# Kernel tuning notes

Measured on AMD Instinct MI355X. Metric: run time of the kernel, lower is better.

## Reference

```python
import jax, jax.numpy as jnp
import numpy as np

BETA = 0.9
THRESHOLD = 1.0
SURROGATE_K = 25.0  # superspike slope

@jax.custom_vjp
def spike(u):
    # Heaviside forward, superspike surrogate gradient
    return (u > 0).astype(u.dtype)

def _spike_fwd(u):
    return spike(u), u

def _spike_bwd(u, g):
    return (g / jnp.square(1.0 + SURROGATE_K * jnp.abs(u)),)

spike.defvjp(_spike_fwd, _spike_bwd)

T, B = 512, 256
VIS_D, IMU_D, TRAJ_D = 256, 64, 64
HID, OUT = 256, 128
FUSE = VIS_D + IMU_D + TRAJ_D  # 384

def setup_inputs() -> dict:
    key = jax.random.key(0)
    ks = jax.random.split(key, 8)
    s_in = 1.0 / np.sqrt(FUSE)
    s_h = 1.0 / np.sqrt(HID)
    return {
        "vis_seq": jax.random.normal(ks[0], (T, B, VIS_D), jnp.float32),
        "imu_seq": jax.random.normal(ks[1], (T, B, IMU_D), jnp.float32),
        "traj_seq": jax.random.normal(ks[2], (T, B, TRAJ_D), jnp.float32),
        "W_in": jax.random.normal(ks[3], (FUSE, HID), jnp.float32) * s_in,
        "b_in": jnp.zeros((HID,), jnp.float32),
        "w_rec": jax.random.normal(ks[4], (HID,), jnp.float32) * 0.1,  # RLIF elementwise recurrent weight
        "W_head": jax.random.normal(ks[5], (HID, OUT), jnp.float32) * s_h,
        "b_head": jnp.zeros((OUT,), jnp.float32),
    }

def reference(vis_seq, imu_seq, traj_seq, W_in, b_in, w_rec, W_head, b_head):
    # fuse latents: [T, B, FUSE]
    fuse_seq = jnp.concatenate([vis_seq, imu_seq, traj_seq], axis=-1)
    # in_proj is time-invariant -> hoist the GEMM out of the scan (same math)
    x_proj = jnp.einsum("tbf,fh->tbh", fuse_seq, W_in) + b_in  # [T, B, HID]
    batch = imu_seq.shape[1]
    V0 = jnp.zeros((batch, HID), x_proj.dtype)
    S0 = jnp.zeros((batch, HID), x_proj.dtype)

    def step(carry, x_t):
        V, S = carry
        # recurrent LIF: leak + input + elementwise recurrent spike feedback
        V = BETA * V + x_t + w_rec * S
        S_new = spike(V - THRESHOLD)
        V = V - S_new * THRESHOLD  # soft reset
        return (V, S_new), S_new

    _, spikes_seq = jax.lax.scan(step, (V0, S0), x_proj)  # [T, B, HID]
    # head is also time-invariant -> single GEMM over the whole sequence
    logits_seq = jnp.einsum("tbh,ho->tbo", spikes_seq, W_head) + b_head  # [T, B, OUT]
    out = jnp.mean(logits_seq, axis=0)  # readout='mean' over time
    return out, logits_seq
```

## Files before the change

kernel.cpp:

```cpp
#include <hip/hip_runtime.h>
#include <hip/hip_bf16.h>
#include <cstdint>

#define T_LEN 512
#define B_SZ  256
#define HID   256
#define OUT   128
#define FUSE  384
#define MROWS (T_LEN * B_SZ)
#define FT    64

typedef _Float16 f16x8 __attribute__((ext_vector_type(8)));
typedef float f32x4 __attribute__((ext_vector_type(4)));

#define PRESC 4096.0f
#define S1    2048.0f
#define S1INV 4.8828125e-4f
#define C0    5.9604644775390625e-8f

#define EPSV  5e-5f

__global__ __launch_bounds__(256) void prep_win(const float* __restrict__ Win,
                                                _Float16* __restrict__ Bpack)
{
  int id = blockIdx.x * 256 + threadIdx.x;
  int img = id >> 10;
  int c = img >> 1, bc = img & 1;
  int slot = id & 1023;
  int s = slot >> 9, sub = (slot >> 6) & 7, pos = slot & 63;
  int fr = pos & 15, fq = pos >> 4;
  int n = bc * 128 + sub * 16 + fr;
  int k0 = c * 32 + fq * 8;
  f16x8 v;
#pragma unroll
  for (int j = 0; j < 8; ++j) {
    float w = Win[(size_t)(k0 + j) * HID + n] * PRESC;
    _Float16 h = (_Float16)w;
    v[j] = (s == 0) ? h : (_Float16)((w - (float)h) * S1);
  }
  *reinterpret_cast<f16x8*>(&Bpack[(size_t)img * 8192 + slot * 8]) = v;
}

__global__ __launch_bounds__(256) void prep_whead(const float* __restrict__ Wh,
                                                  _Float16* __restrict__ Wh3)
{
  int id = blockIdx.x * 256 + threadIdx.x;
  int n = id & 127, kk = (id >> 7) & 31, c = id >> 12;
  Wh3[((size_t)c * 128 + n) * 32 + kk] = (_Float16)Wh[(c * 32 + kk) * OUT + n];
}

__global__ __launch_bounds__(512, 4) void k12_fused(
    const float* __restrict__ vis, const float* __restrict__ imu,
    const float* __restrict__ traj, const _Float16* __restrict__ Bpack,
    const float* __restrict__ bin, const float* __restrict__ wrec,
    uint32_t* __restrict__ sbits, float* __restrict__ scnt)
{
  __shared__ __align__(16) _Float16 Asl[2][4096];
  __shared__ float xt[FT][130];

  const int bid = blockIdx.x;
  const int b   = bid & 255;
  const int hh  = bid >> 8;
  const int tid = threadIdx.x;
  const int wid = tid >> 6, lane = tid & 63;
  const int wr = wid >> 2, wc = wid & 3;
  const int fr = lane & 15, fq = lane >> 4;

  const int arow = (wid & 3) * 16 + fr;
  const int ak   = fq * 8;

  float V = 0.f, S = 0.f, cnt = 0.f, minm = 1e9f;
  const float wrv = (tid < 128) ? wrec[hh * 128 + tid] : 0.f;
  float bvv[2];
  bvv[0] = bin[hh * 128 + wc * 32 + fr];
  bvv[1] = bin[hh * 128 + wc * 32 + 16 + fr];

  float4 a0, a1;
  f16x8 pb0, pb1, pb2, pb3;

  auto loadA = [&](int tc, int c) {
    if (tid < 256) {
      size_t m = (size_t)(tc * FT + arow) * B_SZ + b;
      const float* src; size_t off;
      if (c < 8)       { src = vis;  off = m * 256 + c * 32 + ak; }
      else if (c < 10) { src = imu;  off = m * 64 + (c - 8) * 32 + ak; }
      else             { src = traj; off = m * 64 + (c - 10) * 32 + ak; }
      a0 = *reinterpret_cast<const float4*>(src + off);
      a1 = *reinterpret_cast<const float4*>(src + off + 4);
    }
  };
  auto loadB = [&](int c) {
    const _Float16* base = Bpack + (size_t)(c * 2 + hh) * 8192;
    pb0 = *reinterpret_cast<const f16x8*>(base + (wc * 2 + 0) * 512 + lane * 8);
    pb1 = *reinterpret_cast<const f16x8*>(base + (wc * 2 + 1) * 512 + lane * 8);
    pb2 = *reinterpret_cast<const f16x8*>(base + 4096 + (wc * 2 + 0) * 512 + lane * 8);
    pb3 = *reinterpret_cast<const f16x8*>(base + 4096 + (wc * 2 + 1) * 512 + lane * 8);
  };

  loadA(0, 0); loadB(0);

  for (int tc = 0; tc < 8; ++tc) {
    f32x4 acc0[2][2] = {};
    f32x4 acc1[2][2] = {};

#pragma unroll 1
    for (int c = 0; c < 12; ++c) {
      _Float16* buf = &Asl[c & 1][0];
      if (tid < 256) {
        float av[8] = {a0.x, a0.y, a0.z, a0.w, a1.x, a1.y, a1.z, a1.w};
        f16x8 vh, vl;
#pragma unroll
        for (int j = 0; j < 8; ++j) {
          float w = av[j] * PRESC;
          _Float16 h = (_Float16)w;
          vh[j] = h;
          vl[j] = (_Float16)((w - (float)h) * S1);
        }
        *reinterpret_cast<f16x8*>(&buf[tid * 8])        = vh;
        *reinterpret_cast<f16x8*>(&buf[2048 + tid * 8]) = vl;
      }
      __syncthreads();
      f16x8 bh_0 = pb0, bh_1 = pb1, bl_0 = pb2, bl_1 = pb3;
      if (c + 1 < 12)      { loadA(tc, c + 1); loadB(c + 1); }
      else if (tc + 1 < 8) { loadA(tc + 1, 0); loadB(0); }

#pragma unroll
      for (int mf = 0; mf < 2; ++mf) {
        int sa = wr * 2 + mf;
        f16x8 ah = *reinterpret_cast<const f16x8*>(&buf[sa * 512 + lane * 8]);
        f16x8 al = *reinterpret_cast<const f16x8*>(&buf[2048 + sa * 512 + lane * 8]);
        acc0[mf][0] = __builtin_amdgcn_mfma_f32_16x16x32_f16(ah, bh_0, acc0[mf][0], 0, 0, 0);
        acc1[mf][0] = __builtin_amdgcn_mfma_f32_16x16x32_f16(ah, bl_0, acc1[mf][0], 0, 0, 0);
        acc1[mf][0] = __builtin_amdgcn_mfma_f32_16x16x32_f16(al, bh_0, acc1[mf][0], 0, 0, 0);
        acc0[mf][1] = __builtin_amdgcn_mfma_f32_16x16x32_f16(ah, bh_1, acc0[mf][1], 0, 0, 0);
        acc1[mf][1] = __builtin_amdgcn_mfma_f32_16x16x32_f16(ah, bl_1, acc1[mf][1], 0, 0, 0);
        acc1[mf][1] = __builtin_amdgcn_mfma_f32_16x16x32_f16(al, bh_1, acc1[mf][1], 0, 0, 0);
      }
    }
    __syncthreads();

#pragma unroll
    for (int mf = 0; mf < 2; ++mf)
#pragma unroll
      for (int nf = 0; nf < 2; ++nf) {
        int col = wc * 32 + nf * 16 + fr;
        int rbase = wr * 32 + mf * 16 + fq * 4;
#pragma unroll
        for (int r = 0; r < 4; ++r)
          xt[rbase + r][col] =
              (acc0[mf][nf][r] + acc1[mf][nf][r] * S1INV) * C0 + bvv[nf];
      }
    __syncthreads();

    if (tid < 128) {
#pragma unroll 1
      for (int u0 = 0; u0 < FT; u0 += 8) {
        float xv[8];
#pragma unroll
        for (int u = 0; u < 8; ++u) xv[u] = xt[u0 + u][tid];
#pragma unroll
        for (int u = 0; u < 8; ++u) {
          V = 0.9f * V + xv[u] + wrv * S;
          float d = V - 1.0f;
          float sn = (d > 0.0f) ? 1.0f : 0.0f;
          minm = fminf(minm, fabsf(d));
          V -= sn;
          cnt += sn;
          S = sn;
          unsigned long long mk = __ballot(sn > 0.5f);
          if (lane == 0) {
            int m = (tc * FT + u0 + u) * B_SZ + b;
            int wv = hh * 2 + wid;
            sbits[(size_t)m * 8 + wv * 2 + 0] = (uint32_t)(mk & 0xffffffffull);
            sbits[(size_t)m * 8 + wv * 2 + 1] = (uint32_t)(mk >> 32);
          }
        }
      }
    }
  }

  if (tid < 128)
    scnt[b * HID + hh * 128 + tid] = (minm < EPSV) ? (-cnt - 1.0f) : cnt;
}

#define FSL 12
__global__ __launch_bounds__(512) void k2_fix(
    const float* __restrict__ vis, const float* __restrict__ imu,
    const float* __restrict__ traj, const float* __restrict__ Win,
    const float* __restrict__ bin, const float* __restrict__ wrec,
    uint32_t* __restrict__ sbits, float* __restrict__ scnt)
{
  __shared__ __align__(16) float Wlds[FSL][392];
  __shared__ float xcol[FSL][521];
  __shared__ unsigned char spkb[FSL][516];
  __shared__ int dlist[256];
  __shared__ int nd;

  const int b = blockIdx.x;
  const int tid = threadIdx.x;
  if (tid == 0) nd = 0;
  __syncthreads();
  if (tid < 256) {
    if (scnt[b * HID + tid] < -0.5f) {
      int p = atomicAdd(&nd, 1);
      dlist[p] = tid;
    }
  }
  __syncthreads();
  const int nd0 = nd;
  if (nd0 == 0) return;

  const int t = tid;
  const size_t r = (size_t)t * B_SZ + b;

  for (int sb = 0; sb < nd0; sb += FSL) {
    const int nsb = min(FSL, nd0 - sb);

    for (int idx = tid; idx < FSL * 384; idx += 512) {
      int s = idx / 384, k = idx - s * 384;
      float w = 0.f;
      if (s < nsb) w = Win[(size_t)k * HID + dlist[sb + s]];
      Wlds[s][k] = w;
    }
    __syncthreads();

    float x[FSL];
#pragma unroll
    for (int s = 0; s < FSL; ++s) x[s] = 0.f;

#define SEG(SRC, LEN, DIM, WOFS)                                              \
    {                                                                         \
      const float* src = SRC + r * DIM;                                       \
      _Pragma("unroll 1")                                                     \
      for (int q = 0; q < LEN; q += 4) {                                      \
        float4 a0 = *reinterpret_cast<const float4*>(src + q * 4);            \
        float4 a1 = *reinterpret_cast<const float4*>(src + q * 4 + 4);        \
        float4 a2 = *reinterpret_cast<const float4*>(src + q * 4 + 8);        \
        float4 a3 = *reinterpret_cast<const float4*>(src + q * 4 + 12);       \
        _Pragma("unroll")                                                     \
        for (int s = 0; s < FSL; ++s) {                                       \
          float4 w = *reinterpret_cast<const float4*>(&Wlds[s][WOFS + q * 4]);\
          x[s] += a0.x * w.x; x[s] += a0.y * w.y;                             \
          x[s] += a0.z * w.z; x[s] += a0.w * w.w;                             \
        }                                                                     \
        _Pragma("unroll")                                                     \
        for (int s = 0; s < FSL; ++s) {                                       \
          float4 w = *reinterpret_cast<const float4*>(&Wlds[s][WOFS + q * 4 + 4]); \
          x[s] += a1.x * w.x; x[s] += a1.y * w.y;                             \
          x[s] += a1.z * w.z; x[s] += a1.w * w.w;                             \
        }                                                                     \
        _Pragma("unroll")                                                     \
        for (int s = 0; s < FSL; ++s) {                                       \
          float4 w = *reinterpret_cast<const float4*>(&Wlds[s][WOFS + q * 4 + 8]); \
          x[s] += a2.x * w.x; x[s] += a2.y * w.y;                             \
          x[s] += a2.z * w.z; x[s] += a2.w * w.w;                             \
        }                                                                     \
        _Pragma("unroll")                                                     \
        for (int s = 0; s < FSL; ++s) {                                       \
          float4 w = *reinterpret_cast<const float4*>(&Wlds[s][WOFS + q * 4 + 12]); \
          x[s] += a3.x * w.x; x[s] += a3.y * w.y;                             \
          x[s] += a3.z * w.z; x[s] += a3.w * w.w;                             \
        }                                                                     \
      }                                                                       \
    }

    SEG(vis,  64, 256, 0)
    SEG(imu,  16, 64,  256)
    SEG(traj, 16, 64,  320)
#undef SEG

#pragma unroll
    for (int s = 0; s < FSL; ++s) {
      if (s < nsb) xcol[s][t] = x[s] + bin[dlist[sb + s]];
    }
    __syncthreads();

    if (tid < nsb) {
      const int h = dlist[sb + tid];
      const float mywr = wrec[h];
      float V = 0.f, Sv = 0.f, cnt = 0.f;
#pragma unroll 1
      for (int tt = 0; tt < T_LEN; ++tt) {
        float xv = xcol[tid][tt];
        V = 0.9f * V + xv + mywr * Sv;
        float sn = (V - 1.0f > 0.0f) ? 1.0f : 0.0f;
        V -= sn;
        cnt += sn;
        Sv = sn;
        spkb[tid][tt] = (unsigned char)sn;
      }
      scnt[b * HID + h] = cnt;
    }
    __syncthreads();

    for (int p = tid; p < T_LEN * 8; p += 512) {
      int tt = p >> 3, wv = p & 7;
      uint32_t mc = 0, ms = 0;
      for (int j = 0; j < nsb; ++j) {
        int h = dlist[sb + j];
        if ((h >> 5) == wv) {
          uint32_t bit = 1u << (h & 31);
          mc |= bit;
          if (spkb[j][tt]) ms |= bit;
        }
      }
      if (mc) {
        size_t w = ((size_t)tt * B_SZ + b) * 8 + wv;
        sbits[w] = (sbits[w] & ~mc) | ms;
      }
    }
    __syncthreads();
  }
}

#define LDA 40
__global__ __launch_bounds__(256) void k3_logits(
    const uint32_t* __restrict__ sbits, const _Float16* __restrict__ Wh3,
    const float* __restrict__ bhead, float* __restrict__ logits)
{
  __shared__ __align__(16) _Float16 Sa[128][LDA];
  __shared__ __align__(16) _Float16 Wt[128][LDA];

  const int tid  = threadIdx.x;
  const int brow = blockIdx.x * 128;
  const int srow = tid >> 1, sks = (tid & 1) << 4;
  const int wid = tid >> 6, lane = tid & 63;
  const int wr = wid >> 1, wc = wid & 1;
  const int fr = lane & 15, fq = lane >> 4;

  f32x4 acc[4][4] = {};
  uint32_t wbits;
  uint4 wb0, wb1;

  auto loadS = [&](int c) { wbits = sbits[(size_t)(brow + srow) * 8 + c]; };
  auto loadW = [&](int c) {
    const _Float16* p = Wh3 + ((size_t)c * 128 + srow) * 32 + sks;
    wb0 = *reinterpret_cast<const uint4*>(p);
    wb1 = *reinterpret_cast<const uint4*>(p + 8);
  };

  loadS(0); loadW(0);

  for (int c = 0; c < 8; ++c) {
    __syncthreads();
    {
      f16x8 e0, e1;
#pragma unroll
      for (int j = 0; j < 8; ++j) {
        e0[j] = (_Float16)(float)((wbits >> (sks + j)) & 1u);
        e1[j] = (_Float16)(float)((wbits >> (sks + 8 + j)) & 1u);
      }
      *reinterpret_cast<f16x8*>(&Sa[srow][sks])     = e0;
      *reinterpret_cast<f16x8*>(&Sa[srow][sks + 8]) = e1;
    }
    *reinterpret_cast<uint4*>(&Wt[srow][sks])     = wb0;
    *reinterpret_cast<uint4*>(&Wt[srow][sks + 8]) = wb1;
    __syncthreads();
    if (c + 1 < 8) { loadS(c + 1); loadW(c + 1); }

    f16x8 wf[4];
#pragma unroll
    for (int nf = 0; nf < 4; ++nf)
      wf[nf] = *reinterpret_cast<const f16x8*>(&Wt[wc * 64 + nf * 16 + fr][fq * 8]);
#pragma unroll
    for (int mf = 0; mf < 4; ++mf) {
      f16x8 sf = *reinterpret_cast<const f16x8*>(&Sa[wr * 64 + mf * 16 + fr][fq * 8]);
#pragma unroll
      for (int nf = 0; nf < 4; ++nf)
        acc[mf][nf] = __builtin_amdgcn_mfma_f32_16x16x32_f16(sf, wf[nf], acc[mf][nf], 0, 0, 0);
    }
  }

#pragma unroll
  for (int mf = 0; mf < 4; ++mf)
#pragma unroll
    for (int nf = 0; nf < 4; ++nf) {
      int n = wc * 64 + nf * 16 + fr;
      float bv = bhead[n];
#pragma unroll
      for (int r = 0; r < 4; ++r) {
        int m = brow + wr * 64 + mf * 16 + fq * 4 + r;
        logits[(size_t)m * OUT + n] = acc[mf][nf][r] + bv;
      }
    }
}

__global__ __launch_bounds__(128) void k4_out(
    const float* __restrict__ scnt, const float* __restrict__ Whead,
    const float* __restrict__ bhead, float* __restrict__ outp)
{
  __shared__ float s[HID];
  const int b = blockIdx.x;
  const int o = threadIdx.x;
  s[o] = scnt[b * HID + o];
  s[o + 128] = scnt[b * HID + o + 128];
  __syncthreads();
  float acc = 0.f;
#pragma unroll 8
  for (int h = 0; h < HID; ++h) acc += s[h] * Whead[h * OUT + o];
  outp[b * OUT + o] = acc * (1.0f / (float)T_LEN) + bhead[o];
}

extern "C" void kernel_launch(void* const* d_in, const int* in_sizes, int n_in,
                              void* d_out, int out_size, void* d_ws, size_t ws_size,
                              hipStream_t stream)
{
  const float* vis   = (const float*)d_in[0];
  const float* imu   = (const float*)d_in[1];
  const float* traj  = (const float*)d_in[2];
  const float* Win   = (const float*)d_in[3];
  const float* bin   = (const float*)d_in[4];
  const float* wrec  = (const float*)d_in[5];
  const float* Whead = (const float*)d_in[6];
  const float* bhead = (const float*)d_in[7];

  float* outp   = (float*)d_out;
  float* logits = outp + B_SZ * OUT;

  char* ws = (char*)d_ws;
  const size_t SBITS_B = (size_t)MROWS * 8 * 4;
  const size_t SCNT_B  = (size_t)B_SZ * HID * 4;
  const size_t BPACK_B = (size_t)24 * 8192 * 2;
  uint32_t* sbits = (uint32_t*)ws;
  float*    scnt  = (float*)(ws + SBITS_B);
  _Float16* Bpack = (_Float16*)(ws + SBITS_B + SCNT_B);
  _Float16* Wh3   = (_Float16*)(ws + SBITS_B + SCNT_B + BPACK_B);

  prep_win  <<<dim3(24576 / 256), 256, 0, stream>>>(Win, Bpack);
  prep_whead<<<dim3(32768 / 256), 256, 0, stream>>>(Whead, Wh3);
  k12_fused <<<dim3(512),         512, 0, stream>>>(vis, imu, traj, Bpack, bin,
                                                    wrec, sbits, scnt);
  k2_fix    <<<dim3(B_SZ),        512, 0, stream>>>(vis, imu, traj, Win, bin,
                                                    wrec, sbits, scnt);
  k3_logits <<<dim3(MROWS / 128), 256, 0, stream>>>(sbits, Wh3, bhead, logits);
  k4_out    <<<dim3(B_SZ),        128, 0, stream>>>(scnt, Whead, bhead, outp);
}
```

Measured before the change: 284.3 us.

## Split A-tile staging across two thread groups with two-chunk-deep prefetch

```diff
diff --git a/kernel.cpp b/kernel.cpp
--- a/kernel.cpp
+++ b/kernel.cpp
@@ -63,10 +63,12 @@
   const int hh  = bid >> 8;
   const int tid = threadIdx.x;
   const int wid = tid >> 6, lane = tid & 63;
+  const int grp = tid >> 8;
+  const int stid = tid & 255;
   const int wr = wid >> 2, wc = wid & 3;
   const int fr = lane & 15, fq = lane >> 4;
 
-  const int arow = (wid & 3) * 16 + fr;
+  const int arow = (stid >> 6) * 16 + fr;
   const int ak   = fq * 8;
 
   float V = 0.f, S = 0.f, cnt = 0.f, minm = 1e9f;
@@ -78,18 +80,18 @@
   float4 a0, a1;
   f16x8 pb0, pb1, pb2, pb3;
 
-  auto loadA = [&](int tc, int c) {
-    if (tid < 256) {
-      size_t m = (size_t)(tc * FT + arow) * B_SZ + b;
-      const float* src; size_t off;
-      if (c < 8)       { src = vis;  off = m * 256 + c * 32 + ak; }
-      else if (c < 10) { src = imu;  off = m * 64 + (c - 8) * 32 + ak; }
-      else             { src = traj; off = m * 64 + (c - 10) * 32 + ak; }
-      a0 = *reinterpret_cast<const float4*>(src + off);
-      a1 = *reinterpret_cast<const float4*>(src + off + 4);
-    }
+  auto loadA = [&](int cc) {
+    int tcc = cc / 12, c = cc - tcc * 12;
+    size_t m = (size_t)(tcc * FT + arow) * B_SZ + b;
+    const float* src; size_t off;
+    if (c < 8)       { src = vis;  off = m * 256 + c * 32 + ak; }
+    else if (c < 10) { src = imu;  off = m * 64 + (c - 8) * 32 + ak; }
+    else             { src = traj; off = m * 64 + (c - 10) * 32 + ak; }
+    a0 = *reinterpret_cast<const float4*>(src + off);
+    a1 = *reinterpret_cast<const float4*>(src + off + 4);
   };
-  auto loadB = [&](int c) {
+  auto loadB = [&](int cc) {
+    int c = cc - (cc / 12) * 12;
     const _Float16* base = Bpack + (size_t)(c * 2 + hh) * 8192;
     pb0 = *reinterpret_cast<const f16x8*>(base + (wc * 2 + 0) * 512 + lane * 8);
     pb1 = *reinterpret_cast<const f16x8*>(base + (wc * 2 + 1) * 512 + lane * 8);
@@ -97,82 +99,87 @@
     pb3 = *reinterpret_cast<const f16x8*>(base + 4096 + (wc * 2 + 1) * 512 + lane * 8);
   };
 
-  loadA(0, 0); loadB(0);
-
-  for (int tc = 0; tc < 8; ++tc) {
-    f32x4 acc0[2][2] = {};
-    f32x4 acc1[2][2] = {};
+  loadA(grp);
+  loadB(0);
+
+  f32x4 acc0[2][2] = {};
+  f32x4 acc1[2][2] = {};
 
 #pragma unroll 1
-    for (int c = 0; c < 12; ++c) {
-      _Float16* buf = &Asl[c & 1][0];
-      if (tid < 256) {
-        float av[8] = {a0.x, a0.y, a0.z, a0.w, a1.x, a1.y, a1.z, a1.w};
-        f16x8 vh, vl;
-#pragma unroll
-        for (int j = 0; j < 8; ++j) {
-          float w = av[j] * PRESC;
-          _Float16 h = (_Float16)w;
-          vh[j] = h;
-          vl[j] = (_Float16)((w - (float)h) * S1);
+  for (int cc = 0; cc < 96; ++cc) {
+    _Float16* buf = &Asl[cc & 1][0];
+    const bool mine = (grp == (cc & 1));
+    if (mine) {
+      float av[8] = {a0.x, a0.y, a0.z, a0.w, a1.x, a1.y, a1.z, a1.w};
+      f16x8 vh, vl;
+#pragma unroll
+      for (int j = 0; j < 8; ++j) {
+        float w = av[j] * PRESC;
+        _Float16 h = (_Float16)w;
+        vh[j] = h;
+        vl[j] = (_Float16)((w - (float)h) * S1);
+      }
+      *reinterpret_cast<f16x8*>(&buf[stid * 8])        = vh;
+      *reinterpret_cast<f16x8*>(&buf[2048 + stid * 8]) = vl;
+    }
+    __syncthreads();
+    f16x8 bh_0 = pb0, bh_1 = pb1, bl_0 = pb2, bl_1 = pb3;
+    if (mine && cc + 2 < 96) loadA(cc + 2);
+    if (cc + 1 < 96) loadB(cc + 1);
+
+#pragma unroll
+    for (int mf = 0; mf < 2; ++mf) {
+      int sa = wr * 2 + mf;
+      f16x8 ah = *reinterpret_cast<const f16x8*>(&buf[sa * 512 + lane * 8]);
+      f16x8 al = *reinterpret_cast<const f16x8*>(&buf[2048 + sa * 512 + lane * 8]);
+      acc0[mf][0] = __builtin_amdgcn_mfma_f32_16x16x32_f16(ah, bh_0, acc0[mf][0], 0, 0, 0);
+      acc1[mf][0] = __builtin_amdgcn_mfma_f32_16x16x32_f16(ah, bl_0, acc1[mf][0], 0, 0, 0);
+      acc1[mf][0] = __builtin_amdgcn_mfma_f32_16x16x32_f16(al, bh_0, acc1[mf][0], 0, 0, 0);
+      acc0[mf][1] = __builtin_amdgcn_mfma_f32_16x16x32_f16(ah, bh_1, acc0[mf][1], 0, 0, 0);
+      acc1[mf][1] = __builtin_amdgcn_mfma_f32_16x16x32_f16(ah, bl_1, acc1[mf][1], 0, 0, 0);
+      acc1[mf][1] = __builtin_amdgcn_mfma_f32_16x16x32_f16(al, bh_1, acc1[mf][1], 0, 0, 0);
+    }
+
+    if ((cc - (cc / 12) * 12) == 11) {
+      const int tc = cc / 12;
+      __syncthreads();
+#pragma unroll
+      for (int mf = 0; mf < 2; ++mf)
+#pragma unroll
+        for (int nf = 0; nf < 2; ++nf) {
+          int col = wc * 32 + nf * 16 + fr;
+          int rbase = wr * 32 + mf * 16 + fq * 4;
+#pragma unroll
+          for (int r = 0; r < 4; ++r)
+            xt[rbase + r][col] =
+                (acc0[mf][nf][r] + acc1[mf][nf][r] * S1INV) * C0 + bvv[nf];
+          acc0[mf][nf] = (f32x4){0.f, 0.f, 0.f, 0.f};
+          acc1[mf][nf] = (f32x4){0.f, 0.f, 0.f, 0.f};
         }
-        *reinterpret_cast<f16x8*>(&buf[tid * 8])        = vh;
-        *reinterpret_cast<f16x8*>(&buf[2048 + tid * 8]) = vl;
-      }
       __syncthreads();
-      f16x8 bh_0 = pb0, bh_1 = pb1, bl_0 = pb2, bl_1 = pb3;
-      if (c + 1 < 12)      { loadA(tc, c + 1); loadB(c + 1); }
-      else if (tc + 1 < 8) { loadA(tc + 1, 0); loadB(0); }
-
-#pragma unroll
-      for (int mf = 0; mf < 2; ++mf) {
-        int sa = wr * 2 + mf;
-        f16x8 ah = *reinterpret_cast<const f16x8*>(&buf[sa * 512 + lane * 8]);
-        f16x8 al = *reinterpret_cast<const f16x8*>(&buf[2048 + sa * 512 + lane * 8]);
-        acc0[mf][0] = __builtin_amdgcn_mfma_f32_16x16x32_f16(ah, bh_0, acc0[mf][0], 0, 0, 0);
-        acc1[mf][0] = __builtin_amdgcn_mfma_f32_16x16x32_f16(ah, bl_0, acc1[mf][0], 0, 0, 0);
-        acc1[mf][0] = __builtin_amdgcn_mfma_f32_16x16x32_f16(al, bh_0, acc1[mf][0], 0, 0, 0);
-        acc0[mf][1] = __builtin_amdgcn_mfma_f32_16x16x32_f16(ah, bh_1, acc0[mf][1], 0, 0, 0);
-        acc1[mf][1] = __builtin_amdgcn_mfma_f32_16x16x32_f16(ah, bl_1, acc1[mf][1], 0, 0, 0);
-        acc1[mf][1] = __builtin_amdgcn_mfma_f32_16x16x32_f16(al, bh_1, acc1[mf][1], 0, 0, 0);
-      }
-    }
-    __syncthreads();
-
-#pragma unroll
-    for (int mf = 0; mf < 2; ++mf)
-#pragma unroll
-      for (int nf = 0; nf < 2; ++nf) {
-        int col = wc * 32 + nf * 16 + fr;
-        int rbase = wr * 32 + mf * 16 + fq * 4;
-#pragma unroll
-        for (int r = 0; r < 4; ++r)
-          xt[rbase + r][col] =
-              (acc0[mf][nf][r] + acc1[mf][nf][r] * S1INV) * C0 + bvv[nf];
-      }
-    __syncthreads();
-
-    if (tid < 128) {
+
+      if (tid < 128) {
 #pragma unroll 1
-      for (int u0 = 0; u0 < FT; u0 += 8) {
-        float xv[8];
-#pragma unroll
-        for (int u = 0; u < 8; ++u) xv[u] = xt[u0 + u][tid];
-#pragma unroll
-        for (int u = 0; u < 8; ++u) {
-          V = 0.9f * V + xv[u] + wrv * S;
-          float d = V - 1.0f;
-          float sn = (d > 0.0f) ? 1.0f : 0.0f;
-          minm = fminf(minm, fabsf(d));
-          V -= sn;
-          cnt += sn;
-          S = sn;
-          unsigned long long mk = __ballot(sn > 0.5f);
-          if (lane == 0) {
-            int m = (tc * FT + u0 + u) * B_SZ + b;
-            int wv = hh * 2 + wid;
-            sbits[(size_t)m * 8 + wv * 2 + 0] = (uint32_t)(mk & 0xffffffffull);
-            sbits[(size_t)m * 8 + wv * 2 + 1] = (uint32_t)(mk >> 32);
+        for (int u0 = 0; u0 < FT; u0 += 8) {
+          float xv[8];
+#pragma unroll
+          for (int u = 0; u < 8; ++u) xv[u] = xt[u0 + u][tid];
+#pragma unroll
+          for (int u = 0; u < 8; ++u) {
+            V = 0.9f * V + xv[u] + wrv * S;
+            float d = V - 1.0f;
+            float sn = (d > 0.0f) ? 1.0f : 0.0f;
+            minm = fminf(minm, fabsf(d));
+            V -= sn;
+            cnt += sn;
+            S = sn;
+            unsigned long long mk = __ballot(sn > 0.5f);
+            if (lane == 0) {
+              int m = (tc * FT + u0 + u) * B_SZ + b;
+              int wv = hh * 2 + wid;
+              sbits[(size_t)m * 8 + wv * 2 + 0] = (uint32_t)(mk & 0xffffffffull);
+              sbits[(size_t)m * 8 + wv * 2 + 1] = (uint32_t)(mk >> 32);
+            }
           }
         }
       }
```

New measurement: 277.9 us. -2.2%, faster.

## Use all 512 threads to stage two K-chunks per barrier in fused GEMM

Applied to the files above, without the earlier changes.

```diff
diff --git a/kernel.cpp b/kernel.cpp
--- a/kernel.cpp
+++ b/kernel.cpp
@@ -55,7 +55,7 @@
     const float* __restrict__ bin, const float* __restrict__ wrec,
     uint32_t* __restrict__ sbits, float* __restrict__ scnt)
 {
-  __shared__ __align__(16) _Float16 Asl[2][4096];
+  __shared__ __align__(16) _Float16 Asl[2][8192];
   __shared__ float xt[FT][130];
 
   const int bid = blockIdx.x;
@@ -63,11 +63,13 @@
   const int hh  = bid >> 8;
   const int tid = threadIdx.x;
   const int wid = tid >> 6, lane = tid & 63;
+  const int img  = tid >> 8;
+  const int stid = tid & 255;
   const int wr = wid >> 2, wc = wid & 3;
   const int fr = lane & 15, fq = lane >> 4;
 
-  const int arow = (wid & 3) * 16 + fr;
-  const int ak   = fq * 8;
+  const int arow = (stid >> 6) * 16 + (stid & 15);
+  const int ak   = ((stid & 63) >> 4) * 8;
 
   float V = 0.f, S = 0.f, cnt = 0.f, minm = 1e9f;
   const float wrv = (tid < 128) ? wrec[hh * 128 + tid] : 0.f;
@@ -76,37 +78,39 @@
   bvv[1] = bin[hh * 128 + wc * 32 + 16 + fr];
 
   float4 a0, a1;
-  f16x8 pb0, pb1, pb2, pb3;
+  f16x8 pb[2][4];
 
   auto loadA = [&](int tc, int c) {
-    if (tid < 256) {
-      size_t m = (size_t)(tc * FT + arow) * B_SZ + b;
-      const float* src; size_t off;
-      if (c < 8)       { src = vis;  off = m * 256 + c * 32 + ak; }
-      else if (c < 10) { src = imu;  off = m * 64 + (c - 8) * 32 + ak; }
-      else             { src = traj; off = m * 64 + (c - 10) * 32 + ak; }
-      a0 = *reinterpret_cast<const float4*>(src + off);
-      a1 = *reinterpret_cast<const float4*>(src + off + 4);
-    }
+    size_t m = (size_t)(tc * FT + arow) * B_SZ + b;
+    const float* src; size_t off;
+    if (c < 8)       { src = vis;  off = m * 256 + c * 32 + ak; }
+    else if (c < 10) { src = imu;  off = m * 64 + (c - 8) * 32 + ak; }
+    else             { src = traj; off = m * 64 + (c - 10) * 32 + ak; }
+    a0 = *reinterpret_cast<const float4*>(src + off);
+    a1 = *reinterpret_cast<const float4*>(src + off + 4);
   };
-  auto loadB = [&](int c) {
-    const _Float16* base = Bpack + (size_t)(c * 2 + hh) * 8192;
-    pb0 = *reinterpret_cast<const f16x8*>(base + (wc * 2 + 0) * 512 + lane * 8);
-    pb1 = *reinterpret_cast<const f16x8*>(base + (wc * 2 + 1) * 512 + lane * 8);
-    pb2 = *reinterpret_cast<const f16x8*>(base + 4096 + (wc * 2 + 0) * 512 + lane * 8);
-    pb3 = *reinterpret_cast<const f16x8*>(base + 4096 + (wc * 2 + 1) * 512 + lane * 8);
+  auto loadB = [&](int i) {
+#pragma unroll
+    for (int ii = 0; ii < 2; ++ii) {
+      const _Float16* base = Bpack + (size_t)((2 * i + ii) * 2 + hh) * 8192;
+      pb[ii][0] = *reinterpret_cast<const f16x8*>(base + (wc * 2 + 0) * 512 + lane * 8);
+      pb[ii][1] = *reinterpret_cast<const f16x8*>(base + (wc * 2 + 1) * 512 + lane * 8);
+      pb[ii][2] = *reinterpret_cast<const f16x8*>(base + 4096 + (wc * 2 + 0) * 512 + lane * 8);
+      pb[ii][3] = *reinterpret_cast<const f16x8*>(base + 4096 + (wc * 2 + 1) * 512 + lane * 8);
+    }
   };
 
-  loadA(0, 0); loadB(0);
+  loadA(0, img);
+  loadB(0);
+
+  f32x4 acc0[2][2] = {};
+  f32x4 acc1[2][2] = {};
 
   for (int tc = 0; tc < 8; ++tc) {
-    f32x4 acc0[2][2] = {};
-    f32x4 acc1[2][2] = {};
-
 #pragma unroll 1
-    for (int c = 0; c < 12; ++c) {
-      _Float16* buf = &Asl[c & 1][0];
-      if (tid < 256) {
+    for (int i = 0; i < 6; ++i) {
+      _Float16* buf = &Asl[i & 1][0];
+      {
         float av[8] = {a0.x, a0.y, a0.z, a0.w, a1.x, a1.y, a1.z, a1.w};
         f16x8 vh, vl;
 #pragma unroll
@@ -116,26 +120,29 @@
           vh[j] = h;
           vl[j] = (_Float16)((w - (float)h) * S1);
         }
-        *reinterpret_cast<f16x8*>(&buf[tid * 8])        = vh;
-        *reinterpret_cast<f16x8*>(&buf[2048 + tid * 8]) = vl;
+        *reinterpret_cast<f16x8*>(&buf[img * 4096 + stid * 8])        = vh;
+        *reinterpret_cast<f16x8*>(&buf[img * 4096 + 2048 + stid * 8]) = vl;
       }
       __syncthreads();
-      f16x8 bh_0 = pb0, bh_1 = pb1, bl_0 = pb2, bl_1 = pb3;
-      if (c + 1 < 12)      { loadA(tc, c + 1); loadB(c + 1); }
-      else if (tc + 1 < 8) { loadA(tc + 1, 0); loadB(0); }
-
-#pragma unroll
-      for (int mf = 0; mf < 2; ++mf) {
-        int sa = wr * 2 + mf;
-        f16x8 ah = *reinterpret_cast<const f16x8*>(&buf[sa * 512 + lane * 8]);
-        f16x8 al = *reinterpret_cast<const f16x8*>(&buf[2048 + sa * 512 + lane * 8]);
-        acc0[mf][0] = __builtin_amdgcn_mfma_f32_16x16x32_f16(ah, bh_0, acc0[mf][0], 0, 0, 0);
-        acc1[mf][0] = __builtin_amdgcn_mfma_f32_16x16x32_f16(ah, bl_0, acc1[mf][0], 0, 0, 0);
-        acc1[mf][0] = __builtin_amdgcn_mfma_f32_16x16x32_f16(al, bh_0, acc1[mf][0], 0, 0, 0);
-        acc0[mf][1] = __builtin_amdgcn_mfma_f32_16x16x32_f16(ah, bh_1, acc0[mf][1], 0, 0, 0);
-        acc1[mf][1] = __builtin_amdgcn_mfma_f32_16x16x32_f16(ah, bl_1, acc1[mf][1], 0, 0, 0);
-        acc1[mf][1] = __builtin_amdgcn_mfma_f32_16x16x32_f16(al, bh_1, acc1[mf][1], 0, 0, 0);
-      }
+
+#pragma unroll
+      for (int ii = 0; ii < 2; ++ii) {
+#pragma unroll
+        for (int mf = 0; mf < 2; ++mf) {
+          int sa = wr * 2 + mf;
+          f16x8 ah = *reinterpret_cast<const f16x8*>(&buf[ii * 4096 + sa * 512 + lane * 8]);
+          f16x8 al = *reinterpret_cast<const f16x8*>(&buf[ii * 4096 + 2048 + sa * 512 + lane * 8]);
+          acc0[mf][0] = __builtin_amdgcn_mfma_f32_16x16x32_f16(ah, pb[ii][0], acc0[mf][0], 0, 0, 0);
+          acc1[mf][0] = __builtin_amdgcn_mfma_f32_16x16x32_f16(ah, pb[ii][2], acc1[mf][0], 0, 0, 0);
+          acc1[mf][0] = __builtin_amdgcn_mfma_f32_16x16x32_f16(al, pb[ii][0], acc1[mf][0], 0, 0, 0);
+          acc0[mf][1] = __builtin_amdgcn_mfma_f32_16x16x32_f16(ah, pb[ii][1], acc0[mf][1], 0, 0, 0);
+          acc1[mf][1] = __builtin_amdgcn_mfma_f32_16x16x32_f16(ah, pb[ii][3], acc1[mf][1], 0, 0, 0);
+          acc1[mf][1] = __builtin_amdgcn_mfma_f32_16x16x32_f16(al, pb[ii][1], acc1[mf][1], 0, 0, 0);
+        }
+      }
+
+      if (i + 1 < 6)       { loadA(tc, 2 * (i + 1) + img); loadB(i + 1); }
+      else if (tc + 1 < 8) { loadA(tc + 1, img);           loadB(0); }
     }
     __syncthreads();
 
@@ -149,6 +156,8 @@
         for (int r = 0; r < 4; ++r)
           xt[rbase + r][col] =
               (acc0[mf][nf][r] + acc1[mf][nf][r] * S1INV) * C0 + bvv[nf];
+        acc0[mf][nf] = (f32x4){0.f, 0.f, 0.f, 0.f};
+        acc1[mf][nf] = (f32x4){0.f, 0.f, 0.f, 0.f};
       }
     __syncthreads();
 
```

New measurement: 357.4 us. 1.26x slower.

## Load A fragments directly into registers, drop LDS staging; merge prep kernels

Applied to the files above, without the earlier changes.

```diff
diff --git a/kernel.cpp b/kernel.cpp
--- a/kernel.cpp
+++ b/kernel.cpp
@@ -20,33 +20,34 @@
 
 #define EPSV  5e-5f
 
-__global__ __launch_bounds__(256) void prep_win(const float* __restrict__ Win,
-                                                _Float16* __restrict__ Bpack)
-{
-  int id = blockIdx.x * 256 + threadIdx.x;
-  int img = id >> 10;
-  int c = img >> 1, bc = img & 1;
-  int slot = id & 1023;
-  int s = slot >> 9, sub = (slot >> 6) & 7, pos = slot & 63;
-  int fr = pos & 15, fq = pos >> 4;
-  int n = bc * 128 + sub * 16 + fr;
-  int k0 = c * 32 + fq * 8;
-  f16x8 v;
-#pragma unroll
-  for (int j = 0; j < 8; ++j) {
-    float w = Win[(size_t)(k0 + j) * HID + n] * PRESC;
-    _Float16 h = (_Float16)w;
-    v[j] = (s == 0) ? h : (_Float16)((w - (float)h) * S1);
+__global__ __launch_bounds__(256) void prep_all(const float* __restrict__ Win,
+                                                const float* __restrict__ Wh,
+                                                _Float16* __restrict__ Bpack,
+                                                _Float16* __restrict__ Wh3)
+{
+  int gid = blockIdx.x;
+  if (gid < 96) {
+    int id = gid * 256 + threadIdx.x;
+    int img = id >> 10;
+    int c = img >> 1, bc = img & 1;
+    int slot = id & 1023;
+    int s = slot >> 9, sub = (slot >> 6) & 7, pos = slot & 63;
+    int fr = pos & 15, fq = pos >> 4;
+    int n = bc * 128 + sub * 16 + fr;
+    int k0 = c * 32 + fq * 8;
+    f16x8 v;
+#pragma unroll
+    for (int j = 0; j < 8; ++j) {
+      float w = Win[(size_t)(k0 + j) * HID + n] * PRESC;
+      _Float16 h = (_Float16)w;
+      v[j] = (s == 0) ? h : (_Float16)((w - (float)h) * S1);
+    }
+    *reinterpret_cast<f16x8*>(&Bpack[(size_t)img * 8192 + slot * 8]) = v;
+  } else {
+    int id = (gid - 96) * 256 + threadIdx.x;
+    int n = id & 127, kk = (id >> 7) & 31, c = id >> 12;
+    Wh3[((size_t)c * 128 + n) * 32 + kk] = (_Float16)Wh[(c * 32 + kk) * OUT + n];
   }
-  *reinterpret_cast<f16x8*>(&Bpack[(size_t)img * 8192 + slot * 8]) = v;
-}
-
-__global__ __launch_bounds__(256) void prep_whead(const float* __restrict__ Wh,
-                                                  _Float16* __restrict__ Wh3)
-{
-  int id = blockIdx.x * 256 + threadIdx.x;
-  int n = id & 127, kk = (id >> 7) & 31, c = id >> 12;
-  Wh3[((size_t)c * 128 + n) * 32 + kk] = (_Float16)Wh[(c * 32 + kk) * OUT + n];
 }
 
 __global__ __launch_bounds__(512, 4) void k12_fused(
@@ -55,7 +56,6 @@
     const float* __restrict__ bin, const float* __restrict__ wrec,
     uint32_t* __restrict__ sbits, float* __restrict__ scnt)
 {
-  __shared__ __align__(16) _Float16 Asl[2][4096];
   __shared__ float xt[FT][130];
 
   const int bid = blockIdx.x;
@@ -66,28 +66,27 @@
   const int wr = wid >> 2, wc = wid & 3;
   const int fr = lane & 15, fq = lane >> 4;
 
-  const int arow = (wid & 3) * 16 + fr;
-  const int ak   = fq * 8;
-
   float V = 0.f, S = 0.f, cnt = 0.f, minm = 1e9f;
   const float wrv = (tid < 128) ? wrec[hh * 128 + tid] : 0.f;
   float bvv[2];
   bvv[0] = bin[hh * 128 + wc * 32 + fr];
   bvv[1] = bin[hh * 128 + wc * 32 + 16 + fr];
 
-  float4 a0, a1;
+  float4 pa[4];
   f16x8 pb0, pb1, pb2, pb3;
 
   auto loadA = [&](int tc, int c) {
-    if (tid < 256) {
-      size_t m = (size_t)(tc * FT + arow) * B_SZ + b;
-      const float* src; size_t off;
-      if (c < 8)       { src = vis;  off = m * 256 + c * 32 + ak; }
-      else if (c < 10) { src = imu;  off = m * 64 + (c - 8) * 32 + ak; }
-      else             { src = traj; off = m * 64 + (c - 10) * 32 + ak; }
-      a0 = *reinterpret_cast<const float4*>(src + off);
-      a1 = *reinterpret_cast<const float4*>(src + off + 4);
-    }
+    int row = tc * FT + wr * 32 + fr;
+    size_t m0 = (size_t)row * B_SZ + b;
+    size_t m1 = m0 + (size_t)16 * B_SZ;
+    const float* src; int dim, ko;
+    if (c < 8)       { src = vis;  dim = 256; ko = c * 32 + fq * 8; }
+    else if (c < 10) { src = imu;  dim = 64;  ko = (c - 8) * 32 + fq * 8; }
+    else             { src = traj; dim = 64;  ko = (c - 10) * 32 + fq * 8; }
+    pa[0] = *reinterpret_cast<const float4*>(src + m0 * dim + ko);
+    pa[1] = *reinterpret_cast<const float4*>(src + m0 * dim + ko + 4);
+    pa[2] = *reinterpret_cast<const float4*>(src + m1 * dim + ko);
+    pa[3] = *reinterpret_cast<const float4*>(src + m1 * dim + ko + 4);
   };
   auto loadB = [&](int c) {
     const _Float16* base = Bpack + (size_t)(c * 2 + hh) * 8192;
@@ -105,30 +104,23 @@
 
 #pragma unroll 1
     for (int c = 0; c < 12; ++c) {
-      _Float16* buf = &Asl[c & 1][0];
-      if (tid < 256) {
-        float av[8] = {a0.x, a0.y, a0.z, a0.w, a1.x, a1.y, a1.z, a1.w};
-        f16x8 vh, vl;
+      float4 ca[4] = {pa[0], pa[1], pa[2], pa[3]};
+      f16x8 bh_0 = pb0, bh_1 = pb1, bl_0 = pb2, bl_1 = pb3;
+      if (c + 1 < 12)      { loadA(tc, c + 1); loadB(c + 1); }
+      else if (tc + 1 < 8) { loadA(tc + 1, 0); loadB(0); }
+
+#pragma unroll
+      for (int mf = 0; mf < 2; ++mf) {
+        float av[8] = {ca[2 * mf].x, ca[2 * mf].y, ca[2 * mf].z, ca[2 * mf].w,
+                       ca[2 * mf + 1].x, ca[2 * mf + 1].y, ca[2 * mf + 1].z, ca[2 * mf + 1].w};
+        f16x8 ah, al;
 #pragma unroll
         for (int j = 0; j < 8; ++j) {
           float w = av[j] * PRESC;
           _Float16 h = (_Float16)w;
-          vh[j] = h;
-          vl[j] = (_Float16)((w - (float)h) * S1);
+          ah[j] = h;
+          al[j] = (_Float16)((w - (float)h) * S1);
         }
-        *reinterpret_cast<f16x8*>(&buf[tid * 8])        = vh;
-        *reinterpret_cast<f16x8*>(&buf[2048 + tid * 8]) = vl;
-      }
-      __syncthreads();
-      f16x8 bh_0 = pb0, bh_1 = pb1, bl_0 = pb2, bl_1 = pb3;
-      if (c + 1 < 12)      { loadA(tc, c + 1); loadB(c + 1); }
-      else if (tc + 1 < 8) { loadA(tc + 1, 0); loadB(0); }
-
-#pragma unroll
-      for (int mf = 0; mf < 2; ++mf) {
-        int sa = wr * 2 + mf;
-        f16x8 ah = *reinterpret_cast<const f16x8*>(&buf[sa * 512 + lane * 8]);
-        f16x8 al = *reinterpret_cast<const f16x8*>(&buf[2048 + sa * 512 + lane * 8]);
         acc0[mf][0] = __builtin_amdgcn_mfma_f32_16x16x32_f16(ah, bh_0, acc0[mf][0], 0, 0, 0);
         acc1[mf][0] = __builtin_amdgcn_mfma_f32_16x16x32_f16(ah, bl_0, acc1[mf][0], 0, 0, 0);
         acc1[mf][0] = __builtin_amdgcn_mfma_f32_16x16x32_f16(al, bh_0, acc1[mf][0], 0, 0, 0);
@@ -137,8 +129,8 @@
         acc1[mf][1] = __builtin_amdgcn_mfma_f32_16x16x32_f16(al, bh_1, acc1[mf][1], 0, 0, 0);
       }
     }
-    __syncthreads();
-
+
+    __syncthreads();
 #pragma unroll
     for (int mf = 0; mf < 2; ++mf)
 #pragma unroll
@@ -426,8 +418,7 @@
   _Float16* Bpack = (_Float16*)(ws + SBITS_B + SCNT_B);
   _Float16* Wh3   = (_Float16*)(ws + SBITS_B + SCNT_B + BPACK_B);
 
-  prep_win  <<<dim3(24576 / 256), 256, 0, stream>>>(Win, Bpack);
-  prep_whead<<<dim3(32768 / 256), 256, 0, stream>>>(Whead, Wh3);
+  prep_all  <<<dim3(224),         256, 0, stream>>>(Win, Whead, Bpack, Wh3);
   k12_fused <<<dim3(512),         512, 0, stream>>>(vis, imu, traj, Bpack, bin,
                                                     wrec, sbits, scnt);
   k2_fix    <<<dim3(B_SZ),        512, 0, stream>>>(vis, imu, traj, Win, bin,
```

After: 376.4 us. +32.4%, slower.
